# Optimization experiments

Hardware: AMD Instinct MI355X
Metric: run time of the kernel (lower is better)

The kernel has to match this reference:

```python
import jax, jax.numpy as jnp
import numpy as np

T, B, H, L = 512, 64, 512, 2  # seq len, batch, hidden (=input_size), num_layers


def setup_inputs() -> dict:
    key = jax.random.key(0)
    ks = jax.random.split(key, 8)
    s = 1.0 / np.sqrt(H)  # PyTorch LSTMCell init scale
    return {
        "x": jax.random.normal(ks[0], (T, B, H), dtype=jnp.float32),
        "hx": jax.random.normal(ks[1], (L, B, H), dtype=jnp.float32),
        "cx": jax.random.normal(ks[2], (L, B, H), dtype=jnp.float32),
        "W_ih": jax.random.uniform(ks[3], (L, 4 * H, H), jnp.float32, -s, s),
        "W_hh": jax.random.uniform(ks[4], (L, 4 * H, H), jnp.float32, -s, s),
        "b_ih": jax.random.uniform(ks[5], (L, 4 * H), jnp.float32, -s, s),
        "b_hh": jax.random.uniform(ks[6], (L, 4 * H), jnp.float32, -s, s),
    }


def _lstm_cell(x, h, c, W_ih, W_hh, b_ih, b_hh):
    # gates: [B, 4H], PyTorch gate order i, f, g, o
    gates = x @ W_ih.T + b_ih + h @ W_hh.T + b_hh
    i, f, g, o = jnp.split(gates, 4, axis=-1)
    c_new = jax.nn.sigmoid(f) * c + jax.nn.sigmoid(i) * jnp.tanh(g)
    h_new = jax.nn.sigmoid(o) * jnp.tanh(c_new)
    return h_new, c_new


def reference(x, hx, cx, W_ih, W_hh, b_ih, b_hh):
    num_layers = W_ih.shape[0]

    def step(carry, x_t):
        hs, cs = carry  # each [L, B, H]
        inp = x_t
        new_h, new_c = [], []
        for l in range(num_layers):
            h, c = _lstm_cell(inp, hs[l], cs[l], W_ih[l], W_hh[l], b_ih[l], b_hh[l])
            new_h.append(h)
            new_c.append(c)
            inp = h  # feed current-timestep output to next layer (matches torch code)
        return (jnp.stack(new_h), jnp.stack(new_c)), inp

    (hx_f, cx_f), output = jax.lax.scan(step, (hx, cx), x)
    return output, (hx_f, cx_f)
```

## Files before the change

kernel.cpp:

```cpp
#include <hip/hip_runtime.h>
#include <hip/hip_bf16.h>
#include <stdint.h>

#define Tn 512
#define Bn 64
#define Hn 512
#define LDP 520
#define NWG 128
#define NTHR 512
#define BnHn (Bn * Hn)

typedef unsigned short u16;
typedef unsigned int u32;
typedef unsigned long long u64;
typedef __attribute__((ext_vector_type(8))) short bf16x8;
typedef __attribute__((ext_vector_type(4))) float f32x4;

#define HIST_OFF 16384

__device__ __forceinline__ u16 f2bf(float f) {
  u32 u = __float_as_uint(f);
  u = (u + 0x7FFFu + ((u >> 16) & 1u)) >> 16;
  return (u16)u;
}
__device__ __forceinline__ float sigf(float x) { return 1.f / (1.f + __expf(-x)); }
__device__ __forceinline__ float mytanh(float x) {
  float e = __expf(2.f * x);
  return 1.f - 2.f / (e + 1.f);
}
__device__ __forceinline__ u32 ald32(const u32* p) {
  return __hip_atomic_load(p, __ATOMIC_RELAXED, __HIP_MEMORY_SCOPE_AGENT);
}

extern "C" __global__ void __launch_bounds__(256)
lstm_prep(const float* __restrict__ x, const float* __restrict__ hx,
          u32* __restrict__ ws, int xok, int histok) {
  u16* hist = (u16*)((char*)ws + HIST_OFF);
  u16* xbf  = hist + (size_t)(histok ? 513 : 4) * 2 * BnHn;
  const int slot_init = histok ? 512 : 3;
  const int gt = blockIdx.x * 256 + threadIdx.x;
  if (xok) {
#pragma unroll
    for (int i = 0; i < 8; ++i) {
      const int c = gt + (i << 19);
      const float4 v = *(const float4*)(x + (size_t)c * 4);
      const u64 pk = (u64)((u32)f2bf(v.x) | ((u32)f2bf(v.y) << 16)) |
                     ((u64)((u32)f2bf(v.z) | ((u32)f2bf(v.w) << 16)) << 32);
      *(u64*)(xbf + (size_t)c * 4) = pk;
    }
  }
  if (gt < 32768) {
    const int e0 = 2 * gt;
    const int l = e0 >> 15;
    const int off = e0 & 32767;
    const u32 pk = (u32)f2bf(hx[e0]) | ((u32)f2bf(hx[e0 + 1]) << 16);
    *(u32*)(hist + ((size_t)slot_init * 2 + l) * BnHn + off) = pk;
  }
}

extern "C" __global__ void __launch_bounds__(NTHR, 2)
lstm_fused(const float* __restrict__ x, const float* __restrict__ hx,
           const float* __restrict__ cx, const float* __restrict__ Wih,
           const float* __restrict__ Whh, const float* __restrict__ bih,
           const float* __restrict__ bhh, float* __restrict__ out,
           u32* __restrict__ ws, int xok, int histok) {
  __shared__ u16 sh_inp[32 * LDP];
  __shared__ u16 sh_h[32 * LDP];

  __builtin_amdgcn_fence(__ATOMIC_ACQUIRE, "agent");

  const int wg = blockIdx.x;
  const int tid = threadIdx.x;
  const int layer = wg >> 6;
  const int rem = wg & 63;
  const int shalf = rem >> 5;
  const int cc = rem & 31;
  const int wave = tid >> 6;
  const int lane = tid & 63;
  const int l15 = lane & 15;
  const int lhi = lane >> 4;
  const int mt = wave >> 1;
  const int nt = wave & 1;

  u32* slots = ws;
  u16* hist  = (u16*)((char*)ws + HIST_OFF);
  u16* xbf   = hist + (size_t)(histok ? 513 : 4) * 2 * BnHn;
  const int init_slot = histok ? 512 : 3;

  const int jrow = mt * 16 + l15;
  const int gateA = jrow & 3, colA = jrow >> 2;
  const int growA = gateA * Hn + cc * 16 + colA;
  const float* wihp = Wih + ((size_t)layer * 4 * Hn + growA) * Hn;
  const float* whhp = Whh + ((size_t)layer * 4 * Hn + growA) * Hn;
  bf16x8 wih_f[16], whh_f[16];
#pragma unroll
  for (int kt = 0; kt < 16; ++kt) {
    const int k0 = kt * 32 + lhi * 8;
    const float4 va0 = *(const float4*)(wihp + k0);
    const float4 va1 = *(const float4*)(wihp + k0 + 4);
    const float4 vb0 = *(const float4*)(whhp + k0);
    const float4 vb1 = *(const float4*)(whhp + k0 + 4);
    bf16x8 a, b;
    a[0]=(short)f2bf(va0.x); a[1]=(short)f2bf(va0.y); a[2]=(short)f2bf(va0.z); a[3]=(short)f2bf(va0.w);
    a[4]=(short)f2bf(va1.x); a[5]=(short)f2bf(va1.y); a[6]=(short)f2bf(va1.z); a[7]=(short)f2bf(va1.w);
    b[0]=(short)f2bf(vb0.x); b[1]=(short)f2bf(vb0.y); b[2]=(short)f2bf(vb0.z); b[3]=(short)f2bf(vb0.w);
    b[4]=(short)f2bf(vb1.x); b[5]=(short)f2bf(vb1.y); b[6]=(short)f2bf(vb1.z); b[7]=(short)f2bf(vb1.w);
    wih_f[kt] = a; whh_f[kt] = b;
  }

  const int colE = cc * 16 + mt * 4 + lhi;
  const int sampE = shalf * 32 + nt * 16 + l15;
  float bias[4];
#pragma unroll
  for (int r = 0; r < 4; ++r) {
    const int grow = r * Hn + cc * 16 + mt * 4 + lhi;
    bias[r] = bih[layer * 4 * Hn + grow] + bhh[layer * 4 * Hn + grow];
  }
  float c_cur = cx[((size_t)layer * Bn + sampE) * Hn + colE];

  int pid, tgtoff;
  if (layer == 0) {
    if (lane < 32) { pid = shalf * 32 + lane; tgtoff = 0; }
    else if (histok) { pid = shalf * 32 + (lane - 32); tgtoff = 0; }
    else { pid = 64 + shalf * 32 + (lane - 32); tgtoff = 1; }
  } else {
    if (lane < 32) { pid = 64 + shalf * 32 + lane; tgtoff = 0; }
    else { pid = shalf * 32 + (lane - 32); tgtoff = 1; }
  }
  const u32* pollp = &slots[pid * 16];

  auto stage_x = [&](int t) {
    if (xok) {
      const u16* ip = xbf + ((size_t)t * Bn + shalf * 32) * Hn;
#pragma unroll
      for (int i = 0; i < 4; ++i) {
        const int chunk = tid + i * 512;
        const int row = chunk >> 6, c0 = (chunk & 63) * 8;
        const uint4 v = *(const uint4*)(ip + (size_t)row * Hn + c0);
        *(uint4*)(&sh_inp[row * LDP + c0]) = v;
      }
    } else {
      const float* xp = x + ((size_t)t * Bn + shalf * 32) * Hn;
#pragma unroll
      for (int i = 0; i < 8; ++i) {
        const int chunk = tid + i * 512;
        const int row = chunk >> 7, c0 = (chunk & 127) * 4;
        const float4 v = *(const float4*)(xp + (size_t)row * Hn + c0);
        const u32 p0 = (u32)f2bf(v.x) | ((u32)f2bf(v.y) << 16);
        const u32 p1 = (u32)f2bf(v.z) | ((u32)f2bf(v.w) << 16);
        *(uint2*)(&sh_inp[row * LDP + c0]) = make_uint2(p0, p1);
      }
    }
  };
  auto stage_h = [&](int slot, int srclayer, u16* dst) {
    const u16* hp = hist + ((size_t)slot * 2 + srclayer) * BnHn + (size_t)(shalf * 32) * Hn;
    if (histok) {
#pragma unroll
      for (int i = 0; i < 4; ++i) {
        const int chunk = tid + i * 512;
        const int row = chunk >> 6, c0 = (chunk & 63) * 8;
        const uint4 v = *(const uint4*)(hp + (size_t)row * Hn + c0);
        *(uint4*)(&dst[row * LDP + c0]) = v;
      }
    } else {
#pragma unroll
      for (int i = 0; i < 8; ++i) {
        const int chunk = tid + i * 512;
        const int row = chunk >> 7, c0 = (chunk & 127) * 4;
        const u64 v = __hip_atomic_load((const u64*)(hp + (size_t)row * Hn + c0),
                                        __ATOMIC_RELAXED, __HIP_MEMORY_SCOPE_AGENT);
        *(u64*)(&dst[row * LDP + c0]) = v;
      }
    }
  };
  if (layer == 0) stage_x(0);

  const int smax = Tn + 1;
  u32 ep = 0;
  for (int s = 0; s <= smax; ++s) {
    const int t = layer ? s - 2 : s;
    const bool act = (t >= 0) && (t < Tn);

    if (act) {
      const int slotR = (t == 0) ? init_slot : (histok ? (t - 1) : ((t - 1) & 3));
      stage_h(slotR, layer, sh_h);
      if (layer == 1) {
        const int slotI = histok ? t : (t & 3);
        stage_h(slotI, 0, sh_inp);
      }
    }
    __syncthreads();

    float hn = 0.f, cn = 0.f;
    if (act) {
      f32x4 a0 = {0,0,0,0}, a1 = {0,0,0,0}, b0 = {0,0,0,0}, b1 = {0,0,0,0};
      const int brow = (nt * 16 + l15) * LDP;
#pragma unroll
      for (int kt = 0; kt < 16; kt += 2) {
        const bf16x8 bi0 = *(const bf16x8*)(&sh_inp[brow + kt * 32 + lhi * 8]);
        const bf16x8 bh0 = *(const bf16x8*)(&sh_h[brow + kt * 32 + lhi * 8]);
        const bf16x8 bi1 = *(const bf16x8*)(&sh_inp[brow + (kt + 1) * 32 + lhi * 8]);
        const bf16x8 bh1 = *(const bf16x8*)(&sh_h[brow + (kt + 1) * 32 + lhi * 8]);
        a0 = __builtin_amdgcn_mfma_f32_16x16x32_bf16(wih_f[kt], bi0, a0, 0, 0, 0);
        b0 = __builtin_amdgcn_mfma_f32_16x16x32_bf16(whh_f[kt], bh0, b0, 0, 0, 0);
        a1 = __builtin_amdgcn_mfma_f32_16x16x32_bf16(wih_f[kt + 1], bi1, a1, 0, 0, 0);
        b1 = __builtin_amdgcn_mfma_f32_16x16x32_bf16(whh_f[kt + 1], bh1, b1, 0, 0, 0);
      }
      const float gi = a0[0] + a1[0] + b0[0] + b1[0] + bias[0];
      const float gf = a0[1] + a1[1] + b0[1] + b1[1] + bias[1];
      const float gg = a0[2] + a1[2] + b0[2] + b1[2] + bias[2];
      const float go_ = a0[3] + a1[3] + b0[3] + b1[3] + bias[3];
      cn = sigf(gf) * c_cur + sigf(gi) * mytanh(gg);
      hn = sigf(go_) * mytanh(cn);
      c_cur = cn;

      const u32 hu = (u32)f2bf(hn);
      const u32 pair = hu | (__shfl_xor(hu, 16) << 16);
      const u32 hi2 = __shfl_xor(pair, 32);
      if (lhi == 0) {
        const int slotW = histok ? t : (t & 3);
        const u64 v8 = (u64)pair | ((u64)hi2 << 32);
        u16* wp = hist + ((size_t)slotW * 2 + layer) * BnHn + (size_t)sampE * Hn + cc * 16 + mt * 4;
        __hip_atomic_store((u64*)wp, v8, __ATOMIC_RELAXED, __HIP_MEMORY_SCOPE_AGENT);
      }
    }
    asm volatile("s_waitcnt vmcnt(0)" ::: "memory");
    __syncthreads();
    ++ep;
    if (tid == 0)
      __hip_atomic_store(&slots[wg * 16], ep, __ATOMIC_RELAXED, __HIP_MEMORY_SCOPE_AGENT);

    if (act) {
      if (layer == 1)
        out[((size_t)t * Bn + sampE) * Hn + colE] = hn;
      if (t == Tn - 1) {
        out[(size_t)Tn * Bn * Hn + ((size_t)layer * Bn + sampE) * Hn + colE] = hn;
        out[(size_t)Tn * Bn * Hn + (size_t)2 * Bn * Hn + ((size_t)layer * Bn + sampE) * Hn + colE] = cn;
      }
    }
    if (layer == 0 && (s + 1) < Tn) stage_x(s + 1);

    if (s == smax) break;

    if (wave == 0) {
      while (true) {
        const u32 v = ald32(pollp);
        if (__all((int)(v + (u32)tgtoff >= ep))) break;
      }
    }
    __syncthreads();
    asm volatile("" ::: "memory");
  }
}

extern "C" void kernel_launch(void* const* d_in, const int* in_sizes, int n_in,
                              void* d_out, int out_size, void* d_ws, size_t ws_size,
                              hipStream_t stream) {
  const float* x   = (const float*)d_in[0];
  const float* hx  = (const float*)d_in[1];
  const float* cx  = (const float*)d_in[2];
  const float* Wih = (const float*)d_in[3];
  const float* Whh = (const float*)d_in[4];
  const float* bih = (const float*)d_in[5];
  const float* bhh = (const float*)d_in[6];
  float* outp = (float*)d_out;
  u32* wsp = (u32*)d_ws;

  const size_t slot_bytes = (size_t)2 * Bn * Hn * 2;
  int histok = (ws_size >= HIST_OFF + (size_t)513 * slot_bytes) ? 1 : 0;
  const size_t xoff = HIST_OFF + (size_t)(histok ? 513 : 4) * slot_bytes;
  int xok = (ws_size >= xoff + (size_t)Tn * Bn * Hn * 2) ? 1 : 0;

  hipMemsetAsync(d_ws, 0, HIST_OFF, stream);

  lstm_prep<<<dim3(2048), dim3(256), 0, stream>>>(x, hx, wsp, xok, histok);

  void* args[] = {(void*)&x, (void*)&hx, (void*)&cx, (void*)&Wih, (void*)&Whh,
                  (void*)&bih, (void*)&bhh, (void*)&outp, (void*)&wsp,
                  (void*)&xok, (void*)&histok};
  hipError_t e = hipLaunchCooperativeKernel((const void*)lstm_fused, dim3(NWG),
                                            dim3(NTHR), args, 0, stream);
  if (e != hipSuccess) {
    lstm_fused<<<dim3(NWG), dim3(NTHR), 0, stream>>>(x, hx, cx, Wih, Whh, bih, bhh,
                                                     outp, wsp, xok, histok);
  }
}
```

Before: 1.928 ms.

## Precompute next-step input projection off the recurrent critical path

The input-to-hidden MFMA for the next timestep now runs after the barrier signal and before the poll wait, so only the hidden-to-hidden product sits between the wait and the h write. Layer 1 lags one more step so layer 0's output is ready when it is staged early, and the ring buffer grows from 4 to 8 slots to match. This adds an extra __syncthreads per step and one more pipeline step of latency.

```diff
diff --git a/kernel.cpp b/kernel.cpp
--- a/kernel.cpp
+++ b/kernel.cpp
@@ -36,8 +36,8 @@
 lstm_prep(const float* __restrict__ x, const float* __restrict__ hx,
           u32* __restrict__ ws, int xok, int histok) {
   u16* hist = (u16*)((char*)ws + HIST_OFF);
-  u16* xbf  = hist + (size_t)(histok ? 513 : 4) * 2 * BnHn;
-  const int slot_init = histok ? 512 : 3;
+  u16* xbf  = hist + (size_t)(histok ? 513 : 8) * 2 * BnHn;
+  const int slot_init = histok ? 512 : 7;
   const int gt = blockIdx.x * 256 + threadIdx.x;
   if (xok) {
 #pragma unroll
@@ -84,8 +84,8 @@
 
   u32* slots = ws;
   u16* hist  = (u16*)((char*)ws + HIST_OFF);
-  u16* xbf   = hist + (size_t)(histok ? 513 : 4) * 2 * BnHn;
-  const int init_slot = histok ? 512 : 3;
+  u16* xbf   = hist + (size_t)(histok ? 513 : 8) * 2 * BnHn;
+  const int init_slot = histok ? 512 : 7;
 
   const int jrow = mt * 16 + l15;
   const int gateA = jrow & 3, colA = jrow >> 2;
@@ -173,43 +173,51 @@
       }
     }
   };
+  f32x4 aI0 = {0.f,0.f,0.f,0.f}, aI1 = {0.f,0.f,0.f,0.f};
+  auto compute_aI = [&]() {
+    f32x4 t0 = {0.f,0.f,0.f,0.f}, t1 = {0.f,0.f,0.f,0.f};
+    const int brow = (nt * 16 + l15) * LDP;
+#pragma unroll
+    for (int kt = 0; kt < 16; kt += 2) {
+      const bf16x8 bi0 = *(const bf16x8*)(&sh_inp[brow + kt * 32 + lhi * 8]);
+      const bf16x8 bi1 = *(const bf16x8*)(&sh_inp[brow + (kt + 1) * 32 + lhi * 8]);
+      t0 = __builtin_amdgcn_mfma_f32_16x16x32_bf16(wih_f[kt], bi0, t0, 0, 0, 0);
+      t1 = __builtin_amdgcn_mfma_f32_16x16x32_bf16(wih_f[kt + 1], bi1, t1, 0, 0, 0);
+    }
+    aI0 = t0; aI1 = t1;
+  };
+
   if (layer == 0) stage_x(0);
-
-  const int smax = Tn + 1;
+  __syncthreads();
+  if (layer == 0) compute_aI();
+
+  const int smax = Tn + 2;
   u32 ep = 0;
   for (int s = 0; s <= smax; ++s) {
-    const int t = layer ? s - 2 : s;
+    const int t = layer ? s - 3 : s;
     const bool act = (t >= 0) && (t < Tn);
 
     if (act) {
-      const int slotR = (t == 0) ? init_slot : (histok ? (t - 1) : ((t - 1) & 3));
+      const int slotR = (t == 0) ? init_slot : (histok ? (t - 1) : ((t - 1) & 7));
       stage_h(slotR, layer, sh_h);
-      if (layer == 1) {
-        const int slotI = histok ? t : (t & 3);
-        stage_h(slotI, 0, sh_inp);
-      }
     }
     __syncthreads();
 
     float hn = 0.f, cn = 0.f;
     if (act) {
-      f32x4 a0 = {0,0,0,0}, a1 = {0,0,0,0}, b0 = {0,0,0,0}, b1 = {0,0,0,0};
+      f32x4 b0 = {0,0,0,0}, b1 = {0,0,0,0};
       const int brow = (nt * 16 + l15) * LDP;
 #pragma unroll
       for (int kt = 0; kt < 16; kt += 2) {
-        const bf16x8 bi0 = *(const bf16x8*)(&sh_inp[brow + kt * 32 + lhi * 8]);
         const bf16x8 bh0 = *(const bf16x8*)(&sh_h[brow + kt * 32 + lhi * 8]);
-        const bf16x8 bi1 = *(const bf16x8*)(&sh_inp[brow + (kt + 1) * 32 + lhi * 8]);
         const bf16x8 bh1 = *(const bf16x8*)(&sh_h[brow + (kt + 1) * 32 + lhi * 8]);
-        a0 = __builtin_amdgcn_mfma_f32_16x16x32_bf16(wih_f[kt], bi0, a0, 0, 0, 0);
         b0 = __builtin_amdgcn_mfma_f32_16x16x32_bf16(whh_f[kt], bh0, b0, 0, 0, 0);
-        a1 = __builtin_amdgcn_mfma_f32_16x16x32_bf16(wih_f[kt + 1], bi1, a1, 0, 0, 0);
         b1 = __builtin_amdgcn_mfma_f32_16x16x32_bf16(whh_f[kt + 1], bh1, b1, 0, 0, 0);
       }
-      const float gi = a0[0] + a1[0] + b0[0] + b1[0] + bias[0];
-      const float gf = a0[1] + a1[1] + b0[1] + b1[1] + bias[1];
-      const float gg = a0[2] + a1[2] + b0[2] + b1[2] + bias[2];
-      const float go_ = a0[3] + a1[3] + b0[3] + b1[3] + bias[3];
+      const float gi = aI0[0] + aI1[0] + b0[0] + b1[0] + bias[0];
+      const float gf = aI0[1] + aI1[1] + b0[1] + b1[1] + bias[1];
+      const float gg = aI0[2] + aI1[2] + b0[2] + b1[2] + bias[2];
+      const float go_ = aI0[3] + aI1[3] + b0[3] + b1[3] + bias[3];
       cn = sigf(gf) * c_cur + sigf(gi) * mytanh(gg);
       hn = sigf(go_) * mytanh(cn);
       c_cur = cn;
@@ -218,7 +226,7 @@
       const u32 pair = hu | (__shfl_xor(hu, 16) << 16);
       const u32 hi2 = __shfl_xor(pair, 32);
       if (lhi == 0) {
-        const int slotW = histok ? t : (t & 3);
+        const int slotW = histok ? t : (t & 7);
         const u64 v8 = (u64)pair | ((u64)hi2 << 32);
         u16* wp = hist + ((size_t)slotW * 2 + layer) * BnHn + (size_t)sampE * Hn + cc * 16 + mt * 4;
         __hip_atomic_store((u64*)wp, v8, __ATOMIC_RELAXED, __HIP_MEMORY_SCOPE_AGENT);
@@ -238,7 +246,19 @@
         out[(size_t)Tn * Bn * Hn + (size_t)2 * Bn * Hn + ((size_t)layer * Bn + sampE) * Hn + colE] = cn;
       }
     }
-    if (layer == 0 && (s + 1) < Tn) stage_x(s + 1);
+    bool ihnext = false;
+    if (layer == 0) {
+      if (s + 1 < Tn) { stage_x(s + 1); ihnext = true; }
+    } else {
+      const int u = s - 2;
+      if (u >= 0 && u < Tn) {
+        const int slotI = histok ? u : (u & 7);
+        stage_h(slotI, 0, sh_inp);
+        ihnext = true;
+      }
+    }
+    __syncthreads();
+    if (ihnext) compute_aI();
 
     if (s == smax) break;
 
@@ -268,7 +288,7 @@
 
   const size_t slot_bytes = (size_t)2 * Bn * Hn * 2;
   int histok = (ws_size >= HIST_OFF + (size_t)513 * slot_bytes) ? 1 : 0;
-  const size_t xoff = HIST_OFF + (size_t)(histok ? 513 : 4) * slot_bytes;
+  const size_t xoff = HIST_OFF + (size_t)(histok ? 513 : 8) * slot_bytes;
   int xok = (ws_size >= xoff + (size_t)Tn * Bn * Hn * 2) ? 1 : 0;
 
   hipMemsetAsync(d_ws, 0, HIST_OFF, stream);
```

New measurement: 1.785 ms. 7.4% less time.
